# Performance work log

Measured on AMD Instinct MI355X. Metric: run time of the kernel, lower is better.

## Reference

```python
import jax, jax.numpy as jnp
import numpy as np
from jax import lax

T = 512
DELTA_T = 2.0 ** -10
MAX_RATE = 200.0
DECAY1, DECAY2, CONST, THRESH = 0.25, 0.25, 0.5, 0.3
B = 32


def _conv(x, w):
    # VALID 5x5 conv, stride 1, NCHW / OIHW
    return lax.conv_general_dilated(x, w, (1, 1), 'VALID',
                                    dimension_numbers=('NCHW', 'OIHW', 'NCHW'))


def _avgpool2(x):
    b, c, h, w = x.shape
    return x.reshape(b, c, h // 2, 2, w // 2, 2).mean(axis=(3, 5))


def _lif(drive, mem1, mem2, spike):
    # two-compartment LIF membrane update with soft reset via (1 - spike)
    mem1 = mem1 * DECAY1 * (1.0 - spike) + drive
    mem2 = mem2 * DECAY2 * (1.0 - spike) + CONST * mem1
    new_spike = (mem2 > THRESH).astype(drive.dtype)
    return mem1, mem2, new_spike


def setup_inputs() -> dict:
    key = jax.random.key(0)
    ks = jax.random.split(key, 6)
    image = jax.random.uniform(ks[0], (B, 1, 32, 32), dtype=jnp.float32)
    def kaiming(k, shape, fan_in):
        return jax.random.normal(k, shape, dtype=jnp.float32) / np.float32(np.sqrt(fan_in))
    w1 = kaiming(ks[1], (6, 1, 5, 5), 1 * 25)
    w2 = kaiming(ks[2], (16, 6, 5, 5), 6 * 25)
    w3 = kaiming(ks[3], (120, 16, 5, 5), 16 * 25)
    fw1 = kaiming(ks[4], (84, 120), 120)
    fw2 = kaiming(ks[5], (10, 84), 84)
    return {'image': image, 'w1': w1, 'w2': w2, 'w3': w3, 'fw1': fw1, 'fw2': fw2}


def reference(image, w1, w2, w3, fw1, fw2):
    dt = image.dtype
    z = lambda *s: (jnp.zeros(s, dt), jnp.zeros(s, dt), jnp.zeros(s, dt))
    state0 = (z(B, 6, 28, 28), z(B, 6, 14, 14), z(B, 16, 10, 10),
              z(B, 16, 5, 5), z(B, 120, 1, 1), z(B, 84), z(B, 10),
              jnp.zeros((B, 10), dt))
    keys = jax.random.split(jax.random.key(1), T)

    def step(state, k):
        s1, s2, s3, s4, s5, s6, s7, acc = state
        x = (image * MAX_RATE * DELTA_T > jax.random.uniform(k, image.shape, dtype=dt)).astype(dt)
        s1 = _lif(_conv(x, w1), *s1)
        s2 = _lif(_avgpool2(s1[2]), *s2)
        s3 = _lif(_conv(s2[2], w2), *s3)
        s4 = _lif(_avgpool2(s3[2]), *s4)
        s5 = _lif(_conv(s4[2], w3), *s5)
        s6 = _lif(s5[2].reshape(B, -1) @ fw1.T, *s6)
        s7 = _lif(s6[2] @ fw2.T, *s7)
        acc = acc + s7[2]
        return (s1, s2, s3, s4, s5, s6, s7, acc), None

    final, _ = lax.scan(step, state0, keys)
    return final[-1] / T
```

## Files before the change

### kernel.cpp

```cpp
#include <hip/hip_runtime.h>
#include <cstdint>

#define TSTEPS 512

__device__ __forceinline__ void tfr(uint32_t& x0, uint32_t& x1, int r) {
    x0 += x1;
    x1 = (x1 << r) | (x1 >> (32 - r));
    x1 ^= x0;
}

__device__ __forceinline__ void threefry2x32(uint32_t k0, uint32_t k1,
                                             uint32_t c0, uint32_t c1,
                                             uint32_t& o0, uint32_t& o1) {
    uint32_t k2 = k0 ^ k1 ^ 0x1BD11BDAu;
    uint32_t x0 = c0 + k0, x1 = c1 + k1;
    tfr(x0, x1, 13); tfr(x0, x1, 15); tfr(x0, x1, 26); tfr(x0, x1, 6);
    x0 += k1; x1 += k2 + 1u;
    tfr(x0, x1, 17); tfr(x0, x1, 29); tfr(x0, x1, 16); tfr(x0, x1, 24);
    x0 += k2; x1 += k0 + 2u;
    tfr(x0, x1, 13); tfr(x0, x1, 15); tfr(x0, x1, 26); tfr(x0, x1, 6);
    x0 += k0; x1 += k1 + 3u;
    tfr(x0, x1, 17); tfr(x0, x1, 29); tfr(x0, x1, 16); tfr(x0, x1, 24);
    x0 += k1; x1 += k2 + 4u;
    tfr(x0, x1, 13); tfr(x0, x1, 15); tfr(x0, x1, 26); tfr(x0, x1, 6);
    o0 = x0 + k2; o1 = x1 + k0 + 5u;
}

__global__ void k_keys(uint2* __restrict__ keys) {
    int t = threadIdx.x;
    uint32_t o0, o1;
    threefry2x32(0u, 1u, 0u, (uint32_t)t, o0, o1);
    keys[t] = make_uint2(o0, o1);
}

__global__ __launch_bounds__(256) void k_encode(const float* __restrict__ img,
                                                const uint2* __restrict__ keys,
                                                uint32_t* __restrict__ sxm) {
    int gid = blockIdx.x * 256 + threadIdx.x;
    int t = gid >> 15;
    int n = gid & 32767;
    uint2 k = keys[t];
    uint32_t o0, o1;
    threefry2x32(k.x, k.y, 0u, (uint32_t)n, o0, o1);
    float u = __uint_as_float((o0 >> 9) | 0x3f800000u) - 1.0f;
    float p = (img[n] * 200.0f) * 0.0009765625f;
    unsigned long long bal = __ballot(p > u);
    if ((threadIdx.x & 63) == 0) {
        int word = n >> 5;
        sxm[t * 1024 + word]     = (uint32_t)bal;
        sxm[t * 1024 + word + 1] = (uint32_t)(bal >> 32);
    }
}

__device__ __forceinline__ void lif(float drive, float& m1, float& m2, float& sp) {
    float r = 1.0f - sp;
    m1 = m1 * 0.25f * r + drive;
    m2 = m2 * 0.25f * r + 0.5f * m1;
    sp = (m2 > 0.3f) ? 1.0f : 0.0f;
}

#define SMEM_DW 27542
#define SMEM_BYTES (SMEM_DW * 4)

__global__ __launch_bounds__(1024) void k_main(
        const float* __restrict__ w1g, const float* __restrict__ w2g,
        const float* __restrict__ w3g, const float* __restrict__ fw1g,
        const float* __restrict__ fw2g, const uint32_t* __restrict__ sxm,
        float* __restrict__ out) {
    extern __shared__ float smem[];
    float2*   tbl2v = (float2*)smem;
    float*    tbl1  = smem + 15840;
    float*    fw2s  = smem + 16830;
    float*    s3f   = smem + 17670;
    float*    s4f   = smem + 24070;
    float*    s5f   = smem + 25670;
    float*    s6f   = smem + 26150;
    uint32_t* s1m   = (uint32_t*)(smem + 26486);
    uint32_t* s2m   = (uint32_t*)(smem + 27158);

    const int tid  = threadIdx.x;
    const int lane = tid & 63;
    const int b    = blockIdx.x;

    for (int e = tid; e < 960; e += 1024) {
        int c = e / 160, r = e % 160, ky = r >> 5, m = r & 31;
        float v = 0.0f;
        #pragma unroll
        for (int kx = 0; kx < 5; ++kx)
            if ((m >> kx) & 1) v += w1g[c * 25 + ky * 5 + kx];
        tbl1[(c * 5 + ky) * 33 + m] = v;
    }
    for (int e = tid; e < 7680; e += 1024) {
        int cg = e / 960, r = e % 960, ci = r / 160, r2 = r % 160;
        int ky = r2 >> 5, m = r2 & 31;
        float v0 = 0.0f, v1 = 0.0f;
        #pragma unroll
        for (int kx = 0; kx < 5; ++kx)
            if ((m >> kx) & 1) {
                v0 += w2g[((cg * 2) * 6 + ci) * 25 + ky * 5 + kx];
                v1 += w2g[((cg * 2 + 1) * 6 + ci) * 25 + ky * 5 + kx];
            }
        tbl2v[((cg * 6 + ci) * 5 + ky) * 33 + m] = make_float2(v0, v1);
    }
    for (int e = tid; e < 840; e += 1024) fw2s[e] = fw2g[e];
    for (int e = tid; e < 9872; e += 1024) smem[17670 + e] = 0.0f;

    float fw1r[15];
    if (tid < 672) {
        int o = tid >> 3, j = tid & 7;
        #pragma unroll
        for (int i = 0; i < 15; ++i) fw1r[i] = fw1g[o * 120 + j * 15 + i];
    }

    float m1a[6] = {}, m2a[6] = {}, spa[6] = {};
    float m1b0 = 0, m2b0 = 0, spb0 = 0, m1b1 = 0, m2b1 = 0, spb1 = 0;
    float m1c0 = 0, m2c0 = 0, spc0 = 0, m1c1 = 0, m2c1 = 0, spc1 = 0;
    float m1d = 0, m2d = 0, spd = 0;
    float m1e = 0, m2e = 0, spe = 0;
    float m1f = 0, m2f = 0, spf = 0;
    float m1g = 0, m2g = 0, spg = 0, accf = 0.0f;

    uint32_t sx_cur = 0u, sx_nxt = 0u;
    if (tid < 896) {
        int half = lane >> 5, row = lane & 31;
        sx_cur = sxm[half * 1024 + b * 32 + row];
        sx_nxt = sxm[(half + 2) * 1024 + b * 32 + row];
    }

    __syncthreads();

    #pragma unroll 1
    for (int tau = 0; tau < TSTEPS / 2 + 6; ++tau) {
        const int p = tau & 1, q = p ^ 1;
        float*          s3w0 = s3f + p * 3200;
        float*          s3w1 = s3w0 + 1600;
        const float*    s3r0 = s3f + q * 3200;
        const float*    s3r1 = s3r0 + 1600;
        float*          s4w0 = s4f + p * 800;
        float*          s4w1 = s4w0 + 400;
        const float*    s4r0 = s4f + q * 800;
        const float*    s4r1 = s4r0 + 400;
        float*          s5w0 = s5f + p * 240;
        float*          s5w1 = s5w0 + 120;
        const float*    s5r0 = s5f + q * 240;
        const float*    s5r1 = s5r0 + 120;
        float*          s6w0 = s6f + p * 168;
        float*          s6w1 = s6w0 + 84;
        const float*    s6r0 = s6f + q * 168;
        const float*    s6r1 = s6r0 + 84;
        uint32_t*       s1w0 = s1m + p * 336;
        uint32_t*       s1w1 = s1w0 + 168;
        const uint32_t* s1r0 = s1m + q * 336;
        const uint32_t* s1r1 = s1r0 + 168;
        uint32_t*       s2w0 = s2m + p * 192;
        uint32_t*       s2w1 = s2w0 + 96;
        const uint32_t* s2r0 = s2m + q * 192;
        const uint32_t* s2r1 = s2r0 + 96;

        if (tid < 896) {
            const int y = tid >> 5, x = tid & 31;
            const bool valid = (x < 28);
            #pragma unroll
            for (int u = 0; u < 2; ++u) {
                uint32_t* s1w = u ? s1w1 : s1w0;
                float d[6];
                #pragma unroll
                for (int c = 0; c < 6; ++c) d[c] = 0.0f;
                #pragma unroll
                for (int ky = 0; ky < 5; ++ky) {
                    uint32_t row = (uint32_t)__shfl((int)sx_cur, u * 32 + y + ky, 64);
                    uint32_t mm = (row >> x) & 31u;
                    #pragma unroll
                    for (int c = 0; c < 6; ++c) d[c] += tbl1[(c * 5 + ky) * 33 + mm];
                }
                #pragma unroll
                for (int c = 0; c < 6; ++c) lif(d[c], m1a[c], m2a[c], spa[c]);
                #pragma unroll
                for (int c = 0; c < 6; ++c) {
                    unsigned long long bal = __ballot(valid && (spa[c] > 0.0f));
                    if (lane == 0)       s1w[c * 28 + (tid >> 6) * 2]     = (uint32_t)bal;
                    else if (lane == 32) s1w[c * 28 + (tid >> 6) * 2 + 1] = (uint32_t)(bal >> 32);
                }
            }
            sx_cur = sx_nxt;
            int tt = 2 * tau + 4 + (lane >> 5);
            if (tt > TSTEPS - 1) tt = TSTEPS - 1;
            sx_nxt = sxm[tt * 1024 + b * 32 + (lane & 31)];
        }

        #pragma unroll
        for (int u = 0; u < 2; ++u) {
            const uint32_t* s1r = u ? s1r1 : s1r0;
            uint32_t*       s2w = u ? s2w1 : s2w0;
            {
                const int c = tid / 224, rem = tid % 224;
                const int yy = rem >> 4, xx = rem & 15;
                const bool valid = (xx < 14);
                uint32_t r0 = s1r[c * 28 + 2 * yy];
                uint32_t r1 = s1r[c * 28 + 2 * yy + 1];
                uint32_t sh = 2u * (uint32_t)xx;
                int cnt = (int)((r0 >> sh) & 1u) + (int)((r0 >> (sh + 1)) & 1u)
                        + (int)((r1 >> sh) & 1u) + (int)((r1 >> (sh + 1)) & 1u);
                lif(0.25f * (float)cnt, m1b0, m2b0, spb0);
                unsigned long long bal = __ballot(valid && (spb0 > 0.0f));
                if ((lane & 15) == 0)
                    s2w[tid >> 4] = (uint32_t)((bal >> (lane & 48)) & 0x3FFFull);
            }
            if (tid >= 704) {
                const int slot = tid + 320;
                const int c = slot / 224, rem = slot % 224;
                const int yy = rem >> 4, xx = rem & 15;
                const bool valid = (xx < 14);
                uint32_t r0 = s1r[c * 28 + 2 * yy];
                uint32_t r1 = s1r[c * 28 + 2 * yy + 1];
                uint32_t sh = 2u * (uint32_t)xx;
                int cnt = (int)((r0 >> sh) & 1u) + (int)((r0 >> (sh + 1)) & 1u)
                        + (int)((r1 >> sh) & 1u) + (int)((r1 >> (sh + 1)) & 1u);
                lif(0.25f * (float)cnt, m1b1, m2b1, spb1);
                unsigned long long bal = __ballot(valid && (spb1 > 0.0f));
                if ((lane & 15) == 0)
                    s2w[slot >> 4] = (uint32_t)((bal >> (lane & 48)) & 0x3FFFull);
            }
        }

        if (tid >= 224) {
            const int uu = tid - 224;
            const int px = uu >> 3, cg = uu & 7;
            const int yy = px / 10, xx = px % 10;
            #pragma unroll
            for (int u = 0; u < 2; ++u) {
                const uint32_t* s2r = u ? s2r1 : s2r0;
                float*          s3w = u ? s3w1 : s3w0;
                float d0 = 0.0f, d1 = 0.0f;
                #pragma unroll
                for (int ci = 0; ci < 6; ++ci) {
                    #pragma unroll
                    for (int ky = 0; ky < 5; ++ky) {
                        uint32_t mm = (s2r[ci * 14 + yy + ky] >> xx) & 31u;
                        float2 v = tbl2v[((cg * 6 + ci) * 5 + ky) * 33 + mm];
                        d0 += v.x; d1 += v.y;
                    }
                }
                lif(d0, m1c0, m2c0, spc0);
                lif(d1, m1c1, m2c1, spc1);
                s3w[(cg * 2) * 100 + px]     = spc0;
                s3w[(cg * 2 + 1) * 100 + px] = spc1;
            }
        }

        if (tid < 400) {
            const int c = tid / 25, rem = tid % 25;
            const int yy = rem / 5, xx = rem % 5;
            #pragma unroll
            for (int u = 0; u < 2; ++u) {
                const float* pp = (u ? s3r1 : s3r0) + c * 100 + yy * 20 + xx * 2;
                float sum = pp[0] + pp[1] + pp[10] + pp[11];
                lif(0.25f * sum, m1d, m2d, spd);
                (u ? s4w1 : s4w0)[tid] = spd;
            }
        }

        if (tid < 960) {
            const int cc = tid >> 3, j = tid & 7;
            const float2* wp  = (const float2*)(w3g + cc * 400 + j * 50);
            const float2* sp0 = (const float2*)(s4r0 + j * 50);
            const float2* sp1 = (const float2*)(s4r1 + j * 50);
            float sum0 = 0.0f, sum1 = 0.0f;
            #pragma unroll
            for (int i = 0; i < 25; ++i) {
                float2 w = wp[i];
                float2 a = sp0[i];
                float2 c2 = sp1[i];
                sum0 = fmaf(w.y, a.y,  fmaf(w.x, a.x,  sum0));
                sum1 = fmaf(w.y, c2.y, fmaf(w.x, c2.x, sum1));
            }
            sum0 += __shfl_xor(sum0, 1, 64);
            sum0 += __shfl_xor(sum0, 2, 64);
            sum0 += __shfl_xor(sum0, 4, 64);
            sum1 += __shfl_xor(sum1, 1, 64);
            sum1 += __shfl_xor(sum1, 2, 64);
            sum1 += __shfl_xor(sum1, 4, 64);
            if (j == 0) {
                lif(sum0, m1e, m2e, spe); s5w0[cc] = spe;
                lif(sum1, m1e, m2e, spe); s5w1[cc] = spe;
            }
        }

        if (tid < 672) {
            const int j = tid & 7;
            #pragma unroll
            for (int u = 0; u < 2; ++u) {
                const float* s5r = u ? s5r1 : s5r0;
                float sum = 0.0f;
                #pragma unroll
                for (int i = 0; i < 15; ++i) sum = fmaf(fw1r[i], s5r[j * 15 + i], sum);
                sum += __shfl_xor(sum, 1, 64);
                sum += __shfl_xor(sum, 2, 64);
                sum += __shfl_xor(sum, 4, 64);
                if (j == 0) { lif(sum, m1f, m2f, spf); (u ? s6w1 : s6w0)[tid >> 3] = spf; }
            }
        }

        if (tid < 40) {
            const int o = tid >> 2, j = tid & 3;
            #pragma unroll
            for (int u = 0; u < 2; ++u) {
                const float* s6r = u ? s6r1 : s6r0;
                float sum = 0.0f;
                #pragma unroll
                for (int i = 0; i < 21; ++i)
                    sum = fmaf(fw2s[o * 84 + j * 21 + i], s6r[j * 21 + i], sum);
                sum += __shfl_xor(sum, 1, 64);
                sum += __shfl_xor(sum, 2, 64);
                if (j == 0) { lif(sum, m1g, m2g, spg); accf += spg; }
            }
        }

        __syncthreads();
    }

    if (tid < 40 && (tid & 3) == 0)
        out[b * 10 + (tid >> 2)] = accf * (1.0f / 512.0f);
}

extern "C" void kernel_launch(void* const* d_in, const int* in_sizes, int n_in,
                              void* d_out, int out_size, void* d_ws, size_t ws_size,
                              hipStream_t stream) {
    const float* img = (const float*)d_in[0];
    const float* w1  = (const float*)d_in[1];
    const float* w2  = (const float*)d_in[2];
    const float* w3  = (const float*)d_in[3];
    const float* fw1 = (const float*)d_in[4];
    const float* fw2 = (const float*)d_in[5];
    float* out = (float*)d_out;

    uint2*    keys = (uint2*)d_ws;
    uint32_t* sxm  = (uint32_t*)((char*)d_ws + 4096);

    k_keys<<<1, 512, 0, stream>>>(keys);
    k_encode<<<(TSTEPS * 32768) / 256, 256, 0, stream>>>(img, keys, sxm);

    (void)hipFuncSetAttribute(reinterpret_cast<const void*>(k_main),
                              hipFuncAttributeMaxDynamicSharedMemorySize,
                              SMEM_BYTES);
    k_main<<<32, 1024, SMEM_BYTES, stream>>>(w1, w2, w3, fw1, fw2, sxm, out);
}
```

Baseline: 1.969 ms.

## Pack conv lookup tables into float4/float2 and move fc1 weights to LDS

Measured after the change: 2.490 ms. 26.5% more time.

```diff
diff --git a/kernel.cpp b/kernel.cpp
--- a/kernel.cpp
+++ b/kernel.cpp
@@ -59,7 +59,7 @@
     sp = (m2 > 0.3f) ? 1.0f : 0.0f;
 }
 
-#define SMEM_DW 27542
+#define SMEM_DW 37622
 #define SMEM_BYTES (SMEM_DW * 4)
 
 __global__ __launch_bounds__(1024) void k_main(
@@ -68,53 +68,52 @@
         const float* __restrict__ fw2g, const uint32_t* __restrict__ sxm,
         float* __restrict__ out) {
     extern __shared__ float smem[];
-    float2*   tbl2v = (float2*)smem;
-    float*    tbl1  = smem + 15840;
-    float*    fw2s  = smem + 16830;
-    float*    s3f   = smem + 17670;
-    float*    s4f   = smem + 24070;
-    float*    s5f   = smem + 25670;
-    float*    s6f   = smem + 26150;
-    uint32_t* s1m   = (uint32_t*)(smem + 26486);
-    uint32_t* s2m   = (uint32_t*)(smem + 27158);
+    float4*   tbl2v4 = (float4*)smem;
+    float2*   tbl1p  = (float2*)(smem + 15840);
+    float*    fw2s   = smem + 16830;
+    float*    fw1s   = smem + 17670;
+    float*    s3f    = smem + 27750;
+    float*    s4f    = smem + 34150;
+    float*    s5f    = smem + 35750;
+    float*    s6f    = smem + 36230;
+    uint32_t* s1m    = (uint32_t*)(smem + 36566);
+    uint32_t* s2m    = (uint32_t*)(smem + 37238);
 
     const int tid  = threadIdx.x;
     const int lane = tid & 63;
     const int b    = blockIdx.x;
 
-    for (int e = tid; e < 960; e += 1024) {
-        int c = e / 160, r = e % 160, ky = r >> 5, m = r & 31;
+    for (int e = tid; e < 15840; e += 1024) {
+        int cg = e / 3960, r = e % 3960;
+        int ci = r / 660, r2 = r % 660;
+        int ky = r2 / 132, r3 = r2 % 132;
+        int m = r3 >> 2, qq = r3 & 3;
+        int ch = cg * 4 + qq;
+        float v = 0.0f;
+        #pragma unroll
+        for (int kx = 0; kx < 5; ++kx)
+            if ((m >> kx) & 1) v += w2g[(ch * 6 + ci) * 25 + ky * 5 + kx];
+        smem[e] = v;
+    }
+    for (int e = tid; e < 990; e += 1024) {
+        int pr = e / 330, r = e % 330;
+        int ky = r / 66, r2 = r % 66;
+        int m = r2 >> 1, half = r2 & 1;
+        int c = pr * 2 + half;
         float v = 0.0f;
         #pragma unroll
         for (int kx = 0; kx < 5; ++kx)
             if ((m >> kx) & 1) v += w1g[c * 25 + ky * 5 + kx];
-        tbl1[(c * 5 + ky) * 33 + m] = v;
-    }
-    for (int e = tid; e < 7680; e += 1024) {
-        int cg = e / 960, r = e % 960, ci = r / 160, r2 = r % 160;
-        int ky = r2 >> 5, m = r2 & 31;
-        float v0 = 0.0f, v1 = 0.0f;
-        #pragma unroll
-        for (int kx = 0; kx < 5; ++kx)
-            if ((m >> kx) & 1) {
-                v0 += w2g[((cg * 2) * 6 + ci) * 25 + ky * 5 + kx];
-                v1 += w2g[((cg * 2 + 1) * 6 + ci) * 25 + ky * 5 + kx];
-            }
-        tbl2v[((cg * 6 + ci) * 5 + ky) * 33 + m] = make_float2(v0, v1);
+        smem[15840 + e] = v;
     }
     for (int e = tid; e < 840; e += 1024) fw2s[e] = fw2g[e];
-    for (int e = tid; e < 9872; e += 1024) smem[17670 + e] = 0.0f;
-
-    float fw1r[15];
-    if (tid < 672) {
-        int o = tid >> 3, j = tid & 7;
-        #pragma unroll
-        for (int i = 0; i < 15; ++i) fw1r[i] = fw1g[o * 120 + j * 15 + i];
-    }
+    for (int e = tid; e < 10080; e += 1024) fw1s[e] = fw1g[e];
+    for (int e = tid; e < 9872; e += 1024) smem[27750 + e] = 0.0f;
 
     float m1a[6] = {}, m2a[6] = {}, spa[6] = {};
     float m1b0 = 0, m2b0 = 0, spb0 = 0, m1b1 = 0, m2b1 = 0, spb1 = 0;
     float m1c0 = 0, m2c0 = 0, spc0 = 0, m1c1 = 0, m2c1 = 0, spc1 = 0;
+    float m1c2 = 0, m2c2 = 0, spc2 = 0, m1c3 = 0, m2c3 = 0, spc3 = 0;
     float m1d = 0, m2d = 0, spd = 0;
     float m1e = 0, m2e = 0, spe = 0;
     float m1f = 0, m2f = 0, spf = 0;
@@ -132,37 +131,13 @@
     #pragma unroll 1
     for (int tau = 0; tau < TSTEPS / 2 + 6; ++tau) {
         const int p = tau & 1, q = p ^ 1;
-        float*          s3w0 = s3f + p * 3200;
-        float*          s3w1 = s3w0 + 1600;
-        const float*    s3r0 = s3f + q * 3200;
-        const float*    s3r1 = s3r0 + 1600;
-        float*          s4w0 = s4f + p * 800;
-        float*          s4w1 = s4w0 + 400;
-        const float*    s4r0 = s4f + q * 800;
-        const float*    s4r1 = s4r0 + 400;
-        float*          s5w0 = s5f + p * 240;
-        float*          s5w1 = s5w0 + 120;
-        const float*    s5r0 = s5f + q * 240;
-        const float*    s5r1 = s5r0 + 120;
-        float*          s6w0 = s6f + p * 168;
-        float*          s6w1 = s6w0 + 84;
-        const float*    s6r0 = s6f + q * 168;
-        const float*    s6r1 = s6r0 + 84;
-        uint32_t*       s1w0 = s1m + p * 336;
-        uint32_t*       s1w1 = s1w0 + 168;
-        const uint32_t* s1r0 = s1m + q * 336;
-        const uint32_t* s1r1 = s1r0 + 168;
-        uint32_t*       s2w0 = s2m + p * 192;
-        uint32_t*       s2w1 = s2w0 + 96;
-        const uint32_t* s2r0 = s2m + q * 192;
-        const uint32_t* s2r1 = s2r0 + 96;
 
         if (tid < 896) {
             const int y = tid >> 5, x = tid & 31;
             const bool valid = (x < 28);
             #pragma unroll
             for (int u = 0; u < 2; ++u) {
-                uint32_t* s1w = u ? s1w1 : s1w0;
+                uint32_t* s1w = s1m + p * 336 + u * 168;
                 float d[6];
                 #pragma unroll
                 for (int c = 0; c < 6; ++c) d[c] = 0.0f;
@@ -170,8 +145,12 @@
                 for (int ky = 0; ky < 5; ++ky) {
                     uint32_t row = (uint32_t)__shfl((int)sx_cur, u * 32 + y + ky, 64);
                     uint32_t mm = (row >> x) & 31u;
-                    #pragma unroll
-                    for (int c = 0; c < 6; ++c) d[c] += tbl1[(c * 5 + ky) * 33 + mm];
+                    float2 v0 = tbl1p[(0 * 5 + ky) * 33 + mm];
+                    float2 v1 = tbl1p[(1 * 5 + ky) * 33 + mm];
+                    float2 v2 = tbl1p[(2 * 5 + ky) * 33 + mm];
+                    d[0] += v0.x; d[1] += v0.y;
+                    d[2] += v1.x; d[3] += v1.y;
+                    d[4] += v2.x; d[5] += v2.y;
                 }
                 #pragma unroll
                 for (int c = 0; c < 6; ++c) lif(d[c], m1a[c], m2a[c], spa[c]);
@@ -190,8 +169,8 @@
 
         #pragma unroll
         for (int u = 0; u < 2; ++u) {
-            const uint32_t* s1r = u ? s1r1 : s1r0;
-            uint32_t*       s2w = u ? s2w1 : s2w0;
+            const uint32_t* s1r = s1m + q * 336 + u * 168;
+            uint32_t*       s2w = s2m + p * 192 + u * 96;
             {
                 const int c = tid / 224, rem = tid % 224;
                 const int yy = rem >> 4, xx = rem & 15;
@@ -223,28 +202,33 @@
             }
         }
 
-        if (tid >= 224) {
-            const int uu = tid - 224;
-            const int px = uu >> 3, cg = uu & 7;
+        if (tid >= 624) {
+            const int u2 = tid - 624;
+            const int cg = u2 & 3, px = u2 >> 2;
             const int yy = px / 10, xx = px % 10;
-            #pragma unroll
-            for (int u = 0; u < 2; ++u) {
-                const uint32_t* s2r = u ? s2r1 : s2r0;
-                float*          s3w = u ? s3w1 : s3w0;
-                float d0 = 0.0f, d1 = 0.0f;
+            const float4* tb = tbl2v4 + cg * 990;
+            #pragma unroll
+            for (int u = 0; u < 2; ++u) {
+                const uint32_t* s2r = s2m + q * 192 + u * 96;
+                float*          s3w = s3f + p * 3200 + u * 1600;
+                float d0 = 0.0f, d1 = 0.0f, d2 = 0.0f, d3 = 0.0f;
                 #pragma unroll
                 for (int ci = 0; ci < 6; ++ci) {
                     #pragma unroll
                     for (int ky = 0; ky < 5; ++ky) {
                         uint32_t mm = (s2r[ci * 14 + yy + ky] >> xx) & 31u;
-                        float2 v = tbl2v[((cg * 6 + ci) * 5 + ky) * 33 + mm];
-                        d0 += v.x; d1 += v.y;
+                        float4 v = tb[(ci * 5 + ky) * 33 + mm];
+                        d0 += v.x; d1 += v.y; d2 += v.z; d3 += v.w;
                     }
                 }
                 lif(d0, m1c0, m2c0, spc0);
                 lif(d1, m1c1, m2c1, spc1);
-                s3w[(cg * 2) * 100 + px]     = spc0;
-                s3w[(cg * 2 + 1) * 100 + px] = spc1;
+                lif(d2, m1c2, m2c2, spc2);
+                lif(d3, m1c3, m2c3, spc3);
+                s3w[(cg * 4 + 0) * 100 + px] = spc0;
+                s3w[(cg * 4 + 1) * 100 + px] = spc1;
+                s3w[(cg * 4 + 2) * 100 + px] = spc2;
+                s3w[(cg * 4 + 3) * 100 + px] = spc3;
             }
         }
 
@@ -253,18 +237,18 @@
             const int yy = rem / 5, xx = rem % 5;
             #pragma unroll
             for (int u = 0; u < 2; ++u) {
-                const float* pp = (u ? s3r1 : s3r0) + c * 100 + yy * 20 + xx * 2;
+                const float* pp = s3f + q * 3200 + u * 1600 + c * 100 + yy * 20 + xx * 2;
                 float sum = pp[0] + pp[1] + pp[10] + pp[11];
                 lif(0.25f * sum, m1d, m2d, spd);
-                (u ? s4w1 : s4w0)[tid] = spd;
+                (s4f + p * 800 + u * 400)[tid] = spd;
             }
         }
 
         if (tid < 960) {
             const int cc = tid >> 3, j = tid & 7;
             const float2* wp  = (const float2*)(w3g + cc * 400 + j * 50);
-            const float2* sp0 = (const float2*)(s4r0 + j * 50);
-            const float2* sp1 = (const float2*)(s4r1 + j * 50);
+            const float2* sp0 = (const float2*)(s4f + q * 800 + 0 * 400 + j * 50);
+            const float2* sp1 = (const float2*)(s4f + q * 800 + 1 * 400 + j * 50);
             float sum0 = 0.0f, sum1 = 0.0f;
             #pragma unroll
             for (int i = 0; i < 25; ++i) {
@@ -281,23 +265,24 @@
             sum1 += __shfl_xor(sum1, 2, 64);
             sum1 += __shfl_xor(sum1, 4, 64);
             if (j == 0) {
-                lif(sum0, m1e, m2e, spe); s5w0[cc] = spe;
-                lif(sum1, m1e, m2e, spe); s5w1[cc] = spe;
+                lif(sum0, m1e, m2e, spe); (s5f + p * 240 + 0 * 120)[cc] = spe;
+                lif(sum1, m1e, m2e, spe); (s5f + p * 240 + 1 * 120)[cc] = spe;
             }
         }
 
         if (tid < 672) {
-            const int j = tid & 7;
-            #pragma unroll
-            for (int u = 0; u < 2; ++u) {
-                const float* s5r = u ? s5r1 : s5r0;
+            const int o = tid >> 3, j = tid & 7;
+            const float* wrow = fw1s + o * 120 + j * 15;
+            #pragma unroll
+            for (int u = 0; u < 2; ++u) {
+                const float* s5r = s5f + q * 240 + u * 120;
                 float sum = 0.0f;
                 #pragma unroll
-                for (int i = 0; i < 15; ++i) sum = fmaf(fw1r[i], s5r[j * 15 + i], sum);
+                for (int i = 0; i < 15; ++i) sum = fmaf(wrow[i], s5r[j * 15 + i], sum);
                 sum += __shfl_xor(sum, 1, 64);
                 sum += __shfl_xor(sum, 2, 64);
                 sum += __shfl_xor(sum, 4, 64);
-                if (j == 0) { lif(sum, m1f, m2f, spf); (u ? s6w1 : s6w0)[tid >> 3] = spf; }
+                if (j == 0) { lif(sum, m1f, m2f, spf); (s6f + p * 168 + u * 84)[o] = spf; }
             }
         }
 
@@ -305,7 +290,7 @@
             const int o = tid >> 2, j = tid & 3;
             #pragma unroll
             for (int u = 0; u < 2; ++u) {
-                const float* s6r = u ? s6r1 : s6r0;
+                const float* s6r = s6f + q * 168 + u * 84;
                 float sum = 0.0f;
                 #pragma unroll
                 for (int i = 0; i < 21; ++i)
```
